# Kernel tuning notes

Hardware: AMD Instinct MI355X
Metric: run time of the kernel (lower is better)

Reference implementation:

```python
import jax, jax.numpy as jnp
import numpy as np

B, T, H, S, K = 8, 1024, 8, 64, 31  # batch, time, heads, head_size, kernel_size
C = H * S


def setup_inputs() -> dict:
    key = jax.random.key(0)
    k1, k2, k3 = jax.random.split(key, 3)
    x = jax.random.normal(k1, (B, T, C), dtype=jnp.float32)
    filters = jax.random.normal(k2, (B, T, H * K), dtype=jnp.float32)
    bias = jax.random.normal(k3, (C,), dtype=jnp.float32) * 0.02
    return {"x": x, "filters": filters, "bias": bias}


def reference(x, filters, bias):
    # x: [B,T,C], filters: [B,T,H*K], bias: [C]
    pad = K // 2
    x_pad = jnp.pad(x, ((0, 0), (pad, pad), (0, 0)))  # [B, T+K-1, C]
    idx = jnp.arange(T)[:, None] + jnp.arange(K)[None, :]  # [T,K]
    win = x_pad[:, idx, :]                                  # [B,T,K,C]
    win = win.reshape(B, T, K, H, S)
    # softmax-normalized dynamic kernels per (b,t,h)
    w = jax.nn.softmax(filters.reshape(B, T, H, K), axis=-1)
    out = jnp.einsum('btkhs,bthk->bths', win, w).reshape(B, T, C)
    return out + bias[None, None, :]
```

## Files before the change

kernel.cpp:

```cpp
#include <hip/hip_runtime.h>


#define BB 8
#define TDIM 1024
#define HH 8
#define SS 64
#define KK 31
#define CC (HH * SS)
#define HK (HH * KK)
#define TTILE 64
#define WIN 96
#define PAD 15
#define WSTRIDE 36

__global__ __launch_bounds__(256, 2)
void lightconv_kernel(const float* __restrict__ xg,
                      const float* __restrict__ fg,
                      const float* __restrict__ bg,
                      float* __restrict__ og)
{
    __shared__ float xs[WIN * SS];
    __shared__ float ws[TTILE * WSTRIDE];

    const int t0  = blockIdx.x * TTILE;
    const int h   = blockIdx.y;
    const int b   = blockIdx.z;
    const int tid = threadIdx.x;

    const float* xb = xg + ((size_t)b * TDIM) * CC + h * SS;

    if (blockIdx.x != 0 && blockIdx.x != (TDIM / TTILE - 1)) {
        #pragma unroll
        for (int i = 0; i < 6; ++i) {
            int f  = tid + i * 256;
            int r  = f >> 4;
            int c4 = (f & 15) << 2;
            const float* gp = xb + (size_t)(t0 - PAD + r) * CC + c4;
            __builtin_amdgcn_global_load_lds(
                (const __attribute__((address_space(1))) void*)gp,
                (__attribute__((address_space(3))) void*)&xs[f << 2],
                16, 0, 0);
        }
    } else {
        #pragma unroll
        for (int i = 0; i < 6; ++i) {
            int f  = tid + i * 256;
            int r  = f >> 4;
            int c4 = (f & 15) << 2;
            int t  = t0 - PAD + r;
            float4 v = make_float4(0.f, 0.f, 0.f, 0.f);
            if ((unsigned)t < (unsigned)TDIM)
                v = *reinterpret_cast<const float4*>(xb + (size_t)t * CC + c4);
            *reinterpret_cast<float4*>(&xs[f << 2]) = v;
        }
    }

    {
        const int row  = tid >> 2;
        const int q    = tid & 3;
        const int base = q * 8;
        const float* fp = fg + (size_t)(b * TDIM + t0 + row) * HK + h * KK + base;
        float v[8];
        #pragma unroll
        for (int j = 0; j < 8; ++j)
            v[j] = (base + j < KK) ? fp[j] : -1e30f;
        float m = v[0];
        #pragma unroll
        for (int j = 1; j < 8; ++j) m = fmaxf(m, v[j]);
        m = fmaxf(m, __shfl_xor(m, 1, 4));
        m = fmaxf(m, __shfl_xor(m, 2, 4));
        float s = 0.f;
        #pragma unroll
        for (int j = 0; j < 8; ++j) { v[j] = __expf(v[j] - m); s += v[j]; }
        s += __shfl_xor(s, 1, 4);
        s += __shfl_xor(s, 2, 4);
        float inv = 1.f / s;
        #pragma unroll
        for (int j = 0; j < 8; ++j)
            if (base + j < 32)
                ws[row * WSTRIDE + base + j] = v[j] * inv;
    }
    __syncthreads();

    const int sq = (tid & 15) << 2;
    const int tb = (tid >> 4) << 2;

    float4 xw[35];
    #pragma unroll
    for (int j = 0; j < 35; ++j)
        xw[j] = *reinterpret_cast<const float4*>(&xs[(tb + j) * SS + sq]);

    float4 bias4 = *reinterpret_cast<const float4*>(bg + h * SS + sq);

    float4 acc[4];
    #pragma unroll
    for (int tt = 0; tt < 4; ++tt) acc[tt] = bias4;

    #pragma unroll
    for (int tt = 0; tt < 4; ++tt) {
        #pragma unroll
        for (int kq = 0; kq < 8; ++kq) {
            float4 w4 = *reinterpret_cast<const float4*>(&ws[(tb + tt) * WSTRIDE + (kq << 2)]);
            const float* wv = &w4.x;
            #pragma unroll
            for (int m = 0; m < 4; ++m) {
                float w = wv[m];
                float4 xv = xw[tt + (kq << 2) + m];
                acc[tt].x = fmaf(w, xv.x, acc[tt].x);
                acc[tt].y = fmaf(w, xv.y, acc[tt].y);
                acc[tt].z = fmaf(w, xv.z, acc[tt].z);
                acc[tt].w = fmaf(w, xv.w, acc[tt].w);
            }
        }
    }

    float* ob = og + (size_t)(b * TDIM + t0) * CC + h * SS;
    #pragma unroll
    for (int tt = 0; tt < 4; ++tt)
        *reinterpret_cast<float4*>(ob + (size_t)(tb + tt) * CC + sq) = acc[tt];
}

extern "C" void kernel_launch(void* const* d_in, const int* in_sizes, int n_in,
                              void* d_out, int out_size, void* d_ws, size_t ws_size,
                              hipStream_t stream)
{
    const float* x    = (const float*)d_in[0];
    const float* f    = (const float*)d_in[1];
    const float* bias = (const float*)d_in[2];
    float* out        = (float*)d_out;
    dim3 grid(TDIM / TTILE, HH, BB);
    lightconv_kernel<<<grid, 256, 0, stream>>>(x, f, bias, out);
}
```

Baseline: 81.55 us.

## Process two batches per block with double-buffered LDS prefetch

Halves the grid to 512 blocks, with each block handling two batch indices (b and b+4) for the same time tile and head. The x window and filters for the second batch are staged into a second LDS buffer while the first batch is computed, so global load latency overlaps compute. This doubles LDS use per block, which may lower occupancy, and halves the number of blocks available to spread across CUs.

```diff
diff --git a/kernel.cpp b/kernel.cpp
--- a/kernel.cpp
+++ b/kernel.cpp
@@ -1,17 +1,17 @@
 #include <hip/hip_runtime.h>
 
 
-#define BB 8
 #define TDIM 1024
 #define HH 8
 #define SS 64
 #define KK 31
-#define CC (HH * SS)
-#define HK (HH * KK)
+#define CC 512
+#define HK 248
 #define TTILE 64
 #define WIN 96
 #define PAD 15
 #define WSTRIDE 36
+#define NBLK 512
 
 __global__ __launch_bounds__(256, 2)
 void lightconv_kernel(const float* __restrict__ xg,
@@ -19,51 +19,61 @@
                       const float* __restrict__ bg,
                       float* __restrict__ og)
 {
-    __shared__ float xs[WIN * SS];
-    __shared__ float ws[TTILE * WSTRIDE];
+    __shared__ float xs[2][WIN * SS];
+    __shared__ float ws[2][TTILE * WSTRIDE];
 
-    const int t0  = blockIdx.x * TTILE;
-    const int h   = blockIdx.y;
-    const int b   = blockIdx.z;
     const int tid = threadIdx.x;
 
-    const float* xb = xg + ((size_t)b * TDIM) * CC + h * SS;
+    const int tx = blockIdx.x & 15;
+    const int h  = (blockIdx.x >> 4) & 7;
+    const int b0 = blockIdx.x >> 7;
+    const int t0 = tx * TTILE;
 
-    if (blockIdx.x != 0 && blockIdx.x != (TDIM / TTILE - 1)) {
-        #pragma unroll
-        for (int i = 0; i < 6; ++i) {
-            int f  = tid + i * 256;
-            int r  = f >> 4;
-            int c4 = (f & 15) << 2;
-            const float* gp = xb + (size_t)(t0 - PAD + r) * CC + c4;
-            __builtin_amdgcn_global_load_lds(
-                (const __attribute__((address_space(1))) void*)gp,
-                (__attribute__((address_space(3))) void*)&xs[f << 2],
-                16, 0, 0);
-        }
-    } else {
-        #pragma unroll
-        for (int i = 0; i < 6; ++i) {
-            int f  = tid + i * 256;
-            int r  = f >> 4;
-            int c4 = (f & 15) << 2;
-            int t  = t0 - PAD + r;
-            float4 v = make_float4(0.f, 0.f, 0.f, 0.f);
-            if ((unsigned)t < (unsigned)TDIM)
-                v = *reinterpret_cast<const float4*>(xb + (size_t)t * CC + c4);
-            *reinterpret_cast<float4*>(&xs[f << 2]) = v;
-        }
-    }
+    const int frow  = tid >> 2;
+    const int fbase = (tid & 3) * 8;
 
-    {
-        const int row  = tid >> 2;
-        const int q    = tid & 3;
-        const int base = q * 8;
-        const float* fp = fg + (size_t)(b * TDIM + t0 + row) * HK + h * KK + base;
-        float v[8];
+    const int sq = (tid & 15) << 2;
+    const int tb = (tid >> 4) << 2;
+
+    const bool interior = (tx != 0) && (tx != 15);
+
+    auto load_filters = [&](int b, float* dst) {
+        const float* fp = fg + (size_t)(b * TDIM + t0 + frow) * HK + h * KK + fbase;
         #pragma unroll
         for (int j = 0; j < 8; ++j)
-            v[j] = (base + j < KK) ? fp[j] : -1e30f;
+            dst[j] = (fbase + j < KK) ? fp[j] : -1e30f;
+    };
+
+    auto stage = [&](int b, int buf) {
+        const float* xb = xg + ((size_t)b * TDIM) * CC + h * SS;
+        if (interior) {
+            #pragma unroll
+            for (int i = 0; i < 6; ++i) {
+                int f  = tid + i * 256;
+                int r  = f >> 4;
+                int c4 = (f & 15) << 2;
+                const float* gp = xb + (size_t)(t0 - PAD + r) * CC + c4;
+                __builtin_amdgcn_global_load_lds(
+                    (const __attribute__((address_space(1))) void*)gp,
+                    (__attribute__((address_space(3))) void*)&xs[buf][f << 2],
+                    16, 0, 0);
+            }
+        } else {
+            #pragma unroll
+            for (int i = 0; i < 6; ++i) {
+                int f  = tid + i * 256;
+                int r  = f >> 4;
+                int c4 = (f & 15) << 2;
+                int t  = t0 - PAD + r;
+                float4 v = make_float4(0.f, 0.f, 0.f, 0.f);
+                if ((unsigned)t < (unsigned)TDIM)
+                    v = *reinterpret_cast<const float4*>(xb + (size_t)t * CC + c4);
+                *reinterpret_cast<float4*>(&xs[buf][f << 2]) = v;
+            }
+        }
+    };
+
+    auto softmax_to_lds = [&](int buf, float* v) {
         float m = v[0];
         #pragma unroll
         for (int j = 1; j < 8; ++j) m = fmaxf(m, v[j]);
@@ -77,47 +87,62 @@
         float inv = 1.f / s;
         #pragma unroll
         for (int j = 0; j < 8; ++j)
-            if (base + j < 32)
-                ws[row * WSTRIDE + base + j] = v[j] * inv;
-    }
-    __syncthreads();
-
-    const int sq = (tid & 15) << 2;
-    const int tb = (tid >> 4) << 2;
-
-    float4 xw[35];
-    #pragma unroll
-    for (int j = 0; j < 35; ++j)
-        xw[j] = *reinterpret_cast<const float4*>(&xs[(tb + j) * SS + sq]);
+            if (fbase + j < 32)
+                ws[buf][frow * WSTRIDE + fbase + j] = v[j] * inv;
+    };
 
     float4 bias4 = *reinterpret_cast<const float4*>(bg + h * SS + sq);
 
-    float4 acc[4];
-    #pragma unroll
-    for (int tt = 0; tt < 4; ++tt) acc[tt] = bias4;
+    auto compute_store = [&](int b, int buf) {
+        float4 xw[35];
+        #pragma unroll
+        for (int j = 0; j < 35; ++j)
+            xw[j] = *reinterpret_cast<const float4*>(&xs[buf][(tb + j) * SS + sq]);
 
-    #pragma unroll
-    for (int tt = 0; tt < 4; ++tt) {
+        float4 acc[4];
         #pragma unroll
-        for (int kq = 0; kq < 8; ++kq) {
-            float4 w4 = *reinterpret_cast<const float4*>(&ws[(tb + tt) * WSTRIDE + (kq << 2)]);
-            const float* wv = &w4.x;
+        for (int tt = 0; tt < 4; ++tt) acc[tt] = bias4;
+
+        #pragma unroll
+        for (int tt = 0; tt < 4; ++tt) {
             #pragma unroll
-            for (int m = 0; m < 4; ++m) {
-                float w = wv[m];
-                float4 xv = xw[tt + (kq << 2) + m];
-                acc[tt].x = fmaf(w, xv.x, acc[tt].x);
-                acc[tt].y = fmaf(w, xv.y, acc[tt].y);
-                acc[tt].z = fmaf(w, xv.z, acc[tt].z);
-                acc[tt].w = fmaf(w, xv.w, acc[tt].w);
+            for (int kq = 0; kq < 8; ++kq) {
+                float4 w4 = *reinterpret_cast<const float4*>(
+                    &ws[buf][(tb + tt) * WSTRIDE + (kq << 2)]);
+                const float* wv = &w4.x;
+                #pragma unroll
+                for (int m = 0; m < 4; ++m) {
+                    float w = wv[m];
+                    float4 xv = xw[tt + (kq << 2) + m];
+                    acc[tt].x = fmaf(w, xv.x, acc[tt].x);
+                    acc[tt].y = fmaf(w, xv.y, acc[tt].y);
+                    acc[tt].z = fmaf(w, xv.z, acc[tt].z);
+                    acc[tt].w = fmaf(w, xv.w, acc[tt].w);
+                }
             }
         }
-    }
 
-    float* ob = og + (size_t)(b * TDIM + t0) * CC + h * SS;
-    #pragma unroll
-    for (int tt = 0; tt < 4; ++tt)
-        *reinterpret_cast<float4*>(ob + (size_t)(tb + tt) * CC + sq) = acc[tt];
+        float* ob = og + (size_t)(b * TDIM + t0) * CC + h * SS;
+        #pragma unroll
+        for (int tt = 0; tt < 4; ++tt)
+            *reinterpret_cast<float4*>(ob + (size_t)(tb + tt) * CC + sq) = acc[tt];
+    };
+
+    const int b1 = b0 + 4;
+    float fr0[8], fr1[8];
+
+    load_filters(b0, fr0);
+    stage(b0, 0);
+
+    softmax_to_lds(0, fr0);
+    __syncthreads();
+    stage(b1, 1);
+    load_filters(b1, fr1);
+    compute_store(b0, 0);
+
+    softmax_to_lds(1, fr1);
+    __syncthreads();
+    compute_store(b1, 1);
 }
 
 extern "C" void kernel_launch(void* const* d_in, const int* in_sizes, int n_in,
@@ -128,6 +153,5 @@
     const float* f    = (const float*)d_in[1];
     const float* bias = (const float*)d_in[2];
     float* out        = (float*)d_out;
-    dim3 grid(TDIM / TTILE, HH, BB);
-    lightconv_kernel<<<grid, 256, 0, stream>>>(x, f, bias, out);
+    lightconv_kernel<<<dim3(NBLK), 256, 0, stream>>>(x, f, bias, out);
 }
```

New measurement: 81.80 us. About the same (+0.3%).
